# Performance work log

Hardware: AMD Instinct MI355X
Metric: run time of the kernel (lower is better)

The kernel has to match this reference:

```python
import jax, jax.numpy as jnp
import numpy as np

K = 20
EPS_BN = 1e-5

def knn_idx(x, k):
    # x: [B,N,C] -> k nearest neighbor indices [B,N,k] (self included, as in DGCNN)
    sq = jnp.sum(x * x, axis=-1)                       # [B,N]
    inner = jnp.einsum('bnc,bmc->bnm', x, x)           # [B,N,N]
    neg_dist = 2.0 * inner - sq[:, :, None] - sq[:, None, :]
    _, idx = jax.lax.top_k(neg_dist, k)
    return jax.lax.stop_gradient(idx)

def edge_feat(x, idx):
    # x: [B,N,C], idx: [B,N,k] -> [B,N,k,2C] = cat([x_j - x_i, x_i])
    nbr = jax.vmap(lambda xb, ib: xb[ib])(x, idx)      # [B,N,k,C]
    ctr = jnp.broadcast_to(x[:, :, None, :], nbr.shape)
    return jnp.concatenate([nbr - ctr, ctr], axis=-1)

def edge_conv(x, W, g, b, k):
    e = edge_feat(x, knn_idx(x, k))                    # dynamic kNN graph per layer
    h = jnp.einsum('bnkc,cd->bnkd', e, W)              # 1x1 conv2d
    h = h * (g / jnp.sqrt(1.0 + EPS_BN)) + b           # BN eval (mean=0, var=1)
    return jnp.max(jax.nn.leaky_relu(h, 0.2), axis=2)  # max over neighbors -> [B,N,d]

def layer_norm(x, g, b):
    m = jnp.mean(x, axis=-1, keepdims=True)
    v = jnp.var(x, axis=-1, keepdims=True)
    return (x - m) * jax.lax.rsqrt(v + 1e-5) * g + b

def setup_inputs():
    key = jax.random.key(0)
    B, N = 2, 4096
    ks = jax.random.split(key, 16)
    w = lambda i, shape: jax.random.normal(ks[i], shape, jnp.float32) * 0.05
    ones = lambda d: jnp.ones((d,), jnp.float32)
    zeros = lambda d: jnp.zeros((d,), jnp.float32)
    return dict(
        xyz=jax.random.normal(ks[0], (N, 3), jnp.float32),
        scale=jax.random.normal(ks[1], (N, 3), jnp.float32),
        rot=jax.random.normal(ks[2], (N, 4), jnp.float32),
        opacity=jax.random.normal(ks[3], (N, 1), jnp.float32),
        color=jax.random.normal(ks[4], (N, 3), jnp.float32),
        pose=jax.random.normal(ks[5], (B, 75), jnp.float32),
        lbs_weights=jax.random.normal(ks[6], (N, 24), jnp.float32),
        Wc1=w(7, (226, 64)), g1=ones(64), b1=zeros(64),
        Wc2=w(8, (128, 64)), g2=ones(64), b2=zeros(64),
        Wc3=w(9, (128, 128)), g3=ones(128), b3=zeros(128),
        Wc4=w(10, (256, 256)), g4=ones(256), b4=zeros(256),
        Wc5=w(11, (512, 128)), g5=ones(128), b5=zeros(128),
        Wo1=w(12, (128, 128)), bo1=zeros(128), lg1=ones(128), lb1=zeros(128),
        Wo2=w(13, (128, 128)), bo2=zeros(128), lg2=ones(128), lb2=zeros(128),
        Wo3=w(14, (128, 38)), bo3=zeros(38),
    )

def reference(xyz, scale, rot, opacity, color, pose, lbs_weights,
              Wc1, g1, b1, Wc2, g2, b2, Wc3, g3, b3, Wc4, g4, b4, Wc5, g5, b5,
              Wo1, bo1, lg1, lb1, Wo2, bo2, lg2, lb2, Wo3, bo3):
    B, N = pose.shape[0], xyz.shape[0]
    gfeat = jnp.concatenate([xyz, scale, rot, opacity, color], axis=-1)   # [N,14]
    feats = jnp.concatenate([
        jnp.broadcast_to(gfeat[None], (B, N, gfeat.shape[-1])),
        jnp.broadcast_to(lbs_weights[None], (B, N, lbs_weights.shape[-1])),
        jnp.broadcast_to(pose[:, None, :], (B, N, pose.shape[-1])),
    ], axis=-1)                                                            # [B,N,113]
    # DGCNN graph encoder (dynamic kNN EdgeConv stack)
    x1 = edge_conv(feats, Wc1, g1, b1, K)   # [B,N,64]
    x2 = edge_conv(x1, Wc2, g2, b2, K)      # [B,N,64]
    x3 = edge_conv(x2, Wc3, g3, b3, K)      # [B,N,128]
    x4 = edge_conv(x3, Wc4, g4, b4, K)      # [B,N,256]
    cat = jnp.concatenate([x1, x2, x3, x4], axis=-1)                      # [B,N,512]
    gf = jax.nn.leaky_relu(
        jnp.einsum('bnc,cd->bnd', cat, Wc5) * (g5 / jnp.sqrt(1.0 + EPS_BN)) + b5, 0.2)
    # offset predictor MLP
    h = jax.nn.leaky_relu(layer_norm(gf @ Wo1 + bo1, lg1, lb1), 0.2)
    h = jax.nn.leaky_relu(layer_norm(h @ Wo2 + bo2, lg2, lb2), 0.2)
    off = h @ Wo3 + bo3                                                   # [B,N,38]
    # residual add of gaussian offsets (first 14 dims), lbs offsets raw (last 24)
    out = jnp.concatenate([gfeat[None] + off[..., :14], off[..., 14:]], axis=-1)
    return out                                                            # [B,N,38]
```

## Files before the change

kernel.cpp:

```cpp
#include <hip/hip_runtime.h>
#include <math.h>

#define KNN 20
#define BN_INV 0.9999950000374997f

__device__ __forceinline__ unsigned f2o(float f){
    unsigned u = __float_as_uint(f);
    return (u >> 31) ? ~u : (u | 0x80000000u);
}
__device__ __forceinline__ float o2f(unsigned u){
    return __uint_as_float((u >> 31) ? (u & 0x7fffffffu) : ~u);
}
__device__ __forceinline__ float leaky(float v){ return v > 0.f ? v : 0.2f * v; }

__global__ __launch_bounds__(128) void build_feats_kernel(
    const float* __restrict__ xyz, const float* __restrict__ scale,
    const float* __restrict__ rot, const float* __restrict__ opac,
    const float* __restrict__ color, const float* __restrict__ pose,
    const float* __restrict__ lbs, float* __restrict__ feats,
    float* __restrict__ sqout, int N)
{
    __shared__ float sred[2];
    int row = blockIdx.x;
    int b = row / N, n = row % N;
    int c = threadIdx.x;
    float v = 0.f;
    if      (c <   3) v = xyz  [n*3 + c];
    else if (c <   6) v = scale[n*3 + c-3];
    else if (c <  10) v = rot  [n*4 + c-6];
    else if (c <  11) v = opac [n];
    else if (c <  14) v = color[n*3 + c-11];
    else if (c <  38) v = lbs  [n*24 + c-14];
    else if (c < 113) v = pose [b*75 + c-38];
    if (c < 116) feats[(long)row*116 + c] = v;
    float ss = v * v;
    #pragma unroll
    for (int off = 32; off; off >>= 1) ss += __shfl_xor(ss, off);
    if ((c & 63) == 0) sred[c >> 6] = ss;
    __syncthreads();
    if (c == 0) sqout[row] = sred[0] + sred[1];
}


template<int C>
__global__ __launch_bounds__(256) void dist_gemm_kernel(
    const float* __restrict__ x, int N, int CP, float* __restrict__ G)
{
    __shared__ __align__(16) float smem[9216];
    float (*xi)[36] = (float(*)[36])smem;
    float (*xj)[36] = (float(*)[36])(smem + 128*36);

    const int q = blockIdx.x;
    int bjt = (int)((sqrtf(8.f*(float)q + 1.f) - 1.f) * 0.5f);
    while ((bjt+1)*(bjt+2)/2 <= q) ++bjt;
    while (bjt*(bjt+1)/2 > q) --bjt;
    const int bit = q - bjt*(bjt+1)/2;
    const int bi = bit * 128;
    const int bj = bjt * 128;

    const int b  = blockIdx.z;
    const int t  = threadIdx.x;
    const int tx = t & 15, ty = t >> 4;
    const int CP4 = CP / 4;
    const long base = (long)b * N;
    const float4* xp = (const float4*)x;

    float acc[8][8] = {};

    for (int c0 = 0; c0 < C; c0 += 32){
        const int KC  = (C - c0 < 32) ? (C - c0) : 32;
        const int KC4 = KC >> 2;
        __syncthreads();
        if (KC4 == 8){
            for (int f = t; f < 128 * 8; f += 256){
                int r = f >> 3, c4 = f & 7;
                *(float4*)&xi[r][c4 * 4] = xp[(base + bi + r) * CP4 + (c0 >> 2) + c4];
                *(float4*)&xj[r][c4 * 4] = xp[(base + bj + r) * CP4 + (c0 >> 2) + c4];
            }
        } else {
            for (int f = t; f < 128 * KC4; f += 256){
                int r = f / KC4, c4 = f - r * KC4;
                *(float4*)&xi[r][c4 * 4] = xp[(base + bi + r) * CP4 + (c0 >> 2) + c4];
                *(float4*)&xj[r][c4 * 4] = xp[(base + bj + r) * CP4 + (c0 >> 2) + c4];
            }
        }
        __syncthreads();
        for (int c = 0; c < KC; c += 4){
            float4 A[8], Bv[8];
            #pragma unroll
            for (int ii = 0; ii < 8; ++ii) A[ii]  = *(const float4*)&xi[ty + 16*ii][c];
            #pragma unroll
            for (int jj = 0; jj < 8; ++jj) Bv[jj] = *(const float4*)&xj[tx + 16*jj][c];
            #pragma unroll
            for (int ii = 0; ii < 8; ++ii)
                #pragma unroll
                for (int jj = 0; jj < 8; ++jj){
                    acc[ii][jj] = fmaf(A[ii].x, Bv[jj].x, acc[ii][jj]);
                    acc[ii][jj] = fmaf(A[ii].y, Bv[jj].y, acc[ii][jj]);
                    acc[ii][jj] = fmaf(A[ii].z, Bv[jj].z, acc[ii][jj]);
                    acc[ii][jj] = fmaf(A[ii].w, Bv[jj].w, acc[ii][jj]);
                }
        }
    }

    #pragma unroll
    for (int ii = 0; ii < 8; ++ii){
        long rbase = (base + bi + ty + 16*ii) * N + bj;
        #pragma unroll
        for (int jj = 0; jj < 8; ++jj)
            G[rbase + tx + 16*jj] = acc[ii][jj];
    }

    if (bi != bj){
        float (*tr)[132] = (float(*)[132])smem;
        #pragma unroll
        for (int h = 0; h < 2; ++h){
            __syncthreads();
            #pragma unroll
            for (int ii = 0; ii < 8; ++ii)
                #pragma unroll
                for (int jj = 4*h; jj < 4*h + 4; ++jj)
                    tr[tx + 16*(jj - 4*h)][ty + 16*ii] = acc[ii][jj];
            __syncthreads();
            const int cc = (t & 31) * 4;
            const int r0 = t >> 5;
            #pragma unroll
            for (int f = 0; f < 8; ++f){
                int r = r0 + 8 * f;
                *(float4*)&G[(base + bj + 64*h + r) * N + bi + cc] = *(const float4*)&tr[r][cc];
            }
        }
    }
}

#define TCAP 256
__global__ __launch_bounds__(256) void topk_kernel(
    const float* __restrict__ G, const float* __restrict__ sq,
    int N, int* __restrict__ idx_out)
{
    __shared__ unsigned smax[256];
    __shared__ unsigned cand_u[TCAP];
    __shared__ int      cand_j[TCAP];
    __shared__ unsigned cand_cnt;
    __shared__ unsigned sTu;

    const int row = blockIdx.x;
    const int b   = row >> 12;
    const int t   = threadIdx.x;
    const float4* g4  = (const float4*)(G  + (long)row * 4096);
    const float4* sq4 = (const float4*)(sq + (long)b   * 4096);

    unsigned u[16];
    #pragma unroll
    for (int qq = 0; qq < 4; ++qq){
        int v4 = t + 256 * qq;
        float4 gg = g4[v4];
        float4 ss = sq4[v4];
        u[4*qq+0] = f2o(fmaf(2.f, gg.x, -ss.x));
        u[4*qq+1] = f2o(fmaf(2.f, gg.y, -ss.y));
        u[4*qq+2] = f2o(fmaf(2.f, gg.z, -ss.z));
        u[4*qq+3] = f2o(fmaf(2.f, gg.w, -ss.w));
    }

    unsigned mu = u[0];
    #pragma unroll
    for (int q = 1; q < 16; ++q) mu = u[q] > mu ? u[q] : mu;
    smax[t] = mu;
    if (t == 0) cand_cnt = 0;
    __syncthreads();

    int rank = 0;
    for (int k = 0; k < 256; ++k){
        unsigned ou = smax[k];
        rank += (ou > mu) || (ou == mu && k < t);
    }
    if (rank == KNN - 1) sTu = mu;
    __syncthreads();
    const unsigned Tu = sTu;

    #pragma unroll
    for (int qq = 0; qq < 4; ++qq)
        #pragma unroll
        for (int m = 0; m < 4; ++m){
            int q = 4*qq + m;
            if (u[q] >= Tu){
                unsigned p = atomicAdd(&cand_cnt, 1u);
                if (p < TCAP){ cand_u[p] = u[q]; cand_j[p] = 4*(t + 256*qq) + m; }
            }
        }
    __syncthreads();
    const int cc = (int)cand_cnt;

    if (cc <= TCAP){
        if (t < cc){
            unsigned cu = cand_u[t]; int cj = cand_j[t];
            int r = 0;
            for (int k = 0; k < cc; ++k){
                unsigned ou = cand_u[k];
                r += (ou > cu) || (ou == cu && cand_j[k] < cj);
            }
            if (r < KNN) idx_out[(long)row * KNN + r] = cj;
        }
    } else {
        __shared__ unsigned rv[4]; __shared__ int ri[4]; __shared__ int gj_;
        unsigned lv = 0u; int lj = 0x7fffffff;
        #pragma unroll
        for (int q = 0; q < 16; ++q)
            if (u[q] > lv){ lv = u[q]; lj = 4*(t + 256*(q>>2)) + (q&3); }
        for (int it = 0; it < KNN; ++it){
            unsigned bv = lv; int bj = lj;
            #pragma unroll
            for (int off = 32; off; off >>= 1){
                unsigned ov = __shfl_xor(bv, off);
                int      oj = __shfl_xor(bj, off);
                if (ov > bv || (ov == bv && oj < bj)){ bv = ov; bj = oj; }
            }
            if ((t & 63) == 0){ rv[t >> 6] = bv; ri[t >> 6] = bj; }
            __syncthreads();
            if (t == 0){
                unsigned fv = rv[0]; int fj = ri[0];
                #pragma unroll
                for (int w = 1; w < 4; ++w)
                    if (rv[w] > fv || (rv[w] == fv && ri[w] < fj)){ fv = rv[w]; fj = ri[w]; }
                gj_ = fj;
                idx_out[(long)row * KNN + it] = fj;
            }
            __syncthreads();
            int fj = gj_;
            if (fj >= 0 && ((fj >> 2) & 255) == t){
                u[((fj >> 10) << 2) | (fj & 3)] = 0u;
                lv = 0u; lj = 0x7fffffff;
                #pragma unroll
                for (int q = 0; q < 16; ++q)
                    if (u[q] > lv){ lv = u[q]; lj = 4*(t + 256*(q>>2)) + (q&3); }
            }
            __syncthreads();
        }
    }
}


__device__ __forceinline__ void wcat_emit(const float* __restrict__ W, int C, int D,
                                          int i, float* __restrict__ dst)
{
    int TWOD = 2 * D;
    int c = i / TWOD, n = i - c * TWOD;
    float v = 0.f;
    if (c < C) v = (n < D) ? W[c*D + n] : (W[(C + c)*D + (n - D)] - W[c*D + (n - D)]);
    dst[i] = v;
}

__global__ void prep_all_wcat_kernel(
    const float* __restrict__ Wc1, const float* __restrict__ Wc2,
    const float* __restrict__ Wc3, const float* __restrict__ Wc4,
    float* __restrict__ Wcat)
{
    int i = blockIdx.x * 256 + threadIdx.x;
    if      (i <  14848) wcat_emit(Wc1, 113,  64, i,          Wcat);
    else if (i <  23040) wcat_emit(Wc2,  64,  64, i - 14848,  Wcat + 14848);
    else if (i <  39424) wcat_emit(Wc3,  64, 128, i - 23040,  Wcat + 23040);
    else if (i < 104960) wcat_emit(Wc4, 128, 256, i - 39424,  Wcat + 39424);
}

__global__ __launch_bounds__(256) void gemm_pq_kernel(
    const float* __restrict__ X, int CP, const float* __restrict__ Wcat,
    const float* __restrict__ g, const float* __restrict__ bias,
    int D, int TWOD, float* __restrict__ PQ)
{
    __shared__ __align__(16) float As[128][68];
    __shared__ __align__(16) float Bs[64][132];
    const int bi = blockIdx.x * 128;
    const int bn = blockIdx.y * 128;
    const int t  = threadIdx.x;
    const int tx = t & 15, ty = t >> 4;
    const int CP4 = CP / 4;
    const float4* xp = (const float4*)X;

    float acc[8][8] = {};

    for (int c0 = 0; c0 < CP; c0 += 64){
        const int KC = (CP - c0 < 64) ? (CP - c0) : 64;
        const int KC4 = KC >> 2;
        __syncthreads();
        for (int f = t; f < 128 * KC4; f += 256){
            int r = f / KC4, c4 = f - r * KC4;
            *(float4*)&As[r][c4 * 4] = xp[(long)(bi + r) * CP4 + (c0 >> 2) + c4];
        }
        for (int f = t; f < KC * 32; f += 256){
            int r = f >> 5, c4 = f & 31;
            *(float4*)&Bs[r][c4 * 4] = *(const float4*)&Wcat[(long)(c0 + r) * TWOD + bn + c4 * 4];
        }
        __syncthreads();
        for (int c = 0; c < KC; c += 4){
            float4 A[8];
            #pragma unroll
            for (int ii = 0; ii < 8; ++ii) A[ii] = *(const float4*)&As[ty + 16*ii][c];
            float Bv0[8], Bv1[8], Bv2[8], Bv3[8];
            #pragma unroll
            for (int jj = 0; jj < 8; ++jj){
                Bv0[jj] = Bs[c+0][tx + 16*jj];
                Bv1[jj] = Bs[c+1][tx + 16*jj];
                Bv2[jj] = Bs[c+2][tx + 16*jj];
                Bv3[jj] = Bs[c+3][tx + 16*jj];
            }
            #pragma unroll
            for (int ii = 0; ii < 8; ++ii)
                #pragma unroll
                for (int jj = 0; jj < 8; ++jj){
                    acc[ii][jj] = fmaf(A[ii].x, Bv0[jj], acc[ii][jj]);
                    acc[ii][jj] = fmaf(A[ii].y, Bv1[jj], acc[ii][jj]);
                    acc[ii][jj] = fmaf(A[ii].z, Bv2[jj], acc[ii][jj]);
                    acc[ii][jj] = fmaf(A[ii].w, Bv3[jj], acc[ii][jj]);
                }
        }
    }

    #pragma unroll
    for (int jj = 0; jj < 8; ++jj){
        int n = bn + tx + 16*jj;
        int d = (n < D) ? n : n - D;
        float gg = g[d] * BN_INV;
        float bb = (n < D) ? 0.f : bias[d];
        #pragma unroll
        for (int ii = 0; ii < 8; ++ii)
            PQ[(long)(bi + ty + 16*ii) * TWOD + n] = fmaf(acc[ii][jj], gg, bb);
    }
}

template<int D, int RPB>
__global__ __launch_bounds__(256) void gather_max_kernel(
    const float* __restrict__ PQ, const int* __restrict__ idx, int N,
    float* __restrict__ y, float* __restrict__ sqout)
{
    __shared__ int   lidx[RPB][KNN];
    __shared__ float sred[4];
    const int rb = blockIdx.x * RPB;
    const int t  = threadIdx.x;
    if (t < RPB * KNN) lidx[t / KNN][t % KNN] = idx[(long)rb * KNN + t];
    __syncthreads();

    const int r = t / D, d = t - r * D;
    const int row = rb + r;
    const long base = (long)(row / N) * N;
    const int TWOD = 2 * D;

    float q = PQ[(long)row * TWOD + D + d];
    float m = -INFINITY;
    #pragma unroll
    for (int k = 0; k < KNN; ++k){
        int j = lidx[r][k];
        m = fmaxf(m, PQ[(base + j) * TWOD + d]);
    }
    float val = leaky(m + q);
    y[(long)row * D + d] = val;

    float ss = val * val;
    #pragma unroll
    for (int off = 32; off; off >>= 1) ss += __shfl_xor(ss, off);
    if ((t & 63) == 0) sred[t >> 6] = ss;
    __syncthreads();
    if (d == 0){
        constexpr int WPR = D / 64;
        float s = 0.f;
        int w0 = (r * D) >> 6;
        #pragma unroll
        for (int w = 0; w < WPR; ++w) s += sred[w0 + w];
        sqout[row] = s;
    }
}


__global__ __launch_bounds__(256) void head_gemm1_kernel(
    const float* __restrict__ x1, const float* __restrict__ x2,
    const float* __restrict__ x3, const float* __restrict__ x4,
    const float* __restrict__ Wc5, const float* __restrict__ g5,
    const float* __restrict__ b5, float* __restrict__ gf, int R)
{
    __shared__ __align__(16) float As[64][68];
    __shared__ __align__(16) float Bs[64][68];
    const int bi = blockIdx.x * 64;
    const int bn = blockIdx.y * 64;
    const int t  = threadIdx.x;
    const int tx = t & 15, ty = t >> 4;

    float acc[4][4] = {};

    #pragma unroll 1
    for (int kc = 0; kc < 8; ++kc){
        const float* src; int ld, coff;
        if      (kc == 0){ src = x1; ld = 64;  coff = 0; }
        else if (kc == 1){ src = x2; ld = 64;  coff = 0; }
        else if (kc <  4){ src = x3; ld = 128; coff = (kc-2)*64; }
        else             { src = x4; ld = 256; coff = (kc-4)*64; }
        __syncthreads();
        for (int f = t; f < 64*16; f += 256){
            int r = f >> 4, c4 = f & 15;
            *(float4*)&As[r][c4*4] = *(const float4*)&src[(long)(bi + r)*ld + coff + c4*4];
            *(float4*)&Bs[r][c4*4] = *(const float4*)&Wc5[(long)(kc*64 + r)*128 + bn + c4*4];
        }
        __syncthreads();
        for (int c = 0; c < 64; c += 4){
            float4 A[4];
            #pragma unroll
            for (int ii = 0; ii < 4; ++ii) A[ii] = *(const float4*)&As[ty + 16*ii][c];
            float B0[4], B1[4], B2[4], B3[4];
            #pragma unroll
            for (int jj = 0; jj < 4; ++jj){
                B0[jj] = Bs[c+0][tx + 16*jj];
                B1[jj] = Bs[c+1][tx + 16*jj];
                B2[jj] = Bs[c+2][tx + 16*jj];
                B3[jj] = Bs[c+3][tx + 16*jj];
            }
            #pragma unroll
            for (int ii = 0; ii < 4; ++ii)
                #pragma unroll
                for (int jj = 0; jj < 4; ++jj){
                    acc[ii][jj] = fmaf(A[ii].x, B0[jj], acc[ii][jj]);
                    acc[ii][jj] = fmaf(A[ii].y, B1[jj], acc[ii][jj]);
                    acc[ii][jj] = fmaf(A[ii].z, B2[jj], acc[ii][jj]);
                    acc[ii][jj] = fmaf(A[ii].w, B3[jj], acc[ii][jj]);
                }
        }
    }

    #pragma unroll
    for (int jj = 0; jj < 4; ++jj){
        int n = bn + tx + 16*jj;
        float gg = g5[n] * BN_INV, bb = b5[n];
        #pragma unroll
        for (int ii = 0; ii < 4; ++ii)
            gf[(long)(bi + ty + 16*ii)*128 + n] = leaky(fmaf(acc[ii][jj], gg, bb));
    }
}

__global__ __launch_bounds__(256) void head_lngemm_kernel(
    const float* __restrict__ hin, const float* __restrict__ W,
    const float* __restrict__ bo, const float* __restrict__ lg,
    const float* __restrict__ lb, float* __restrict__ hout, int R)
{
    __shared__ __align__(16) float As[64][68];
    __shared__ __align__(16) float Bs[64][132];
    const int bi = blockIdx.x * 64;
    const int t  = threadIdx.x;
    const int tx = t & 15, ty = t >> 4;

    float acc[4][8] = {};

    #pragma unroll 1
    for (int kc = 0; kc < 2; ++kc){
        __syncthreads();
        for (int f = t; f < 64*16; f += 256){
            int r = f >> 4, c4 = f & 15;
            *(float4*)&As[r][c4*4] = *(const float4*)&hin[(long)(bi + r)*128 + kc*64 + c4*4];
        }
        for (int f = t; f < 64*32; f += 256){
            int r = f >> 5, c4 = f & 31;
            *(float4*)&Bs[r][c4*4] = *(const float4*)&W[(long)(kc*64 + r)*128 + c4*4];
        }
        __syncthreads();
        for (int c = 0; c < 64; c += 4){
            float4 A[4];
            #pragma unroll
            for (int ii = 0; ii < 4; ++ii) A[ii] = *(const float4*)&As[ty + 16*ii][c];
            float B0[8], B1[8], B2[8], B3[8];
            #pragma unroll
            for (int jj = 0; jj < 8; ++jj){
                B0[jj] = Bs[c+0][tx + 16*jj];
                B1[jj] = Bs[c+1][tx + 16*jj];
                B2[jj] = Bs[c+2][tx + 16*jj];
                B3[jj] = Bs[c+3][tx + 16*jj];
            }
            #pragma unroll
            for (int ii = 0; ii < 4; ++ii)
                #pragma unroll
                for (int jj = 0; jj < 8; ++jj){
                    acc[ii][jj] = fmaf(A[ii].x, B0[jj], acc[ii][jj]);
                    acc[ii][jj] = fmaf(A[ii].y, B1[jj], acc[ii][jj]);
                    acc[ii][jj] = fmaf(A[ii].z, B2[jj], acc[ii][jj]);
                    acc[ii][jj] = fmaf(A[ii].w, B3[jj], acc[ii][jj]);
                }
        }
    }

    float bon[8], lgn[8], lbn[8];
    #pragma unroll
    for (int jj = 0; jj < 8; ++jj){
        int n = tx + 16*jj;
        bon[jj] = bo[n]; lgn[jj] = lg[n]; lbn[jj] = lb[n];
    }
    #pragma unroll
    for (int ii = 0; ii < 4; ++ii){
        float s1 = 0.f, s2 = 0.f;
        #pragma unroll
        for (int jj = 0; jj < 8; ++jj){
            float a = acc[ii][jj] + bon[jj];
            acc[ii][jj] = a;
            s1 += a; s2 += a*a;
        }
        #pragma unroll
        for (int off = 8; off; off >>= 1){
            s1 += __shfl_xor(s1, off);
            s2 += __shfl_xor(s2, off);
        }
        float m = s1 * (1.f/128.f);
        float v = s2 * (1.f/128.f) - m*m;
        float rinv = rsqrtf(v + 1e-5f);
        long r = bi + ty + 16*ii;
        #pragma unroll
        for (int jj = 0; jj < 8; ++jj)
            hout[r*128 + tx + 16*jj] = leaky((acc[ii][jj] - m) * rinv * lgn[jj] + lbn[jj]);
    }
}

#define OP 16
__global__ __launch_bounds__(256) void head_out_kernel(
    const float* __restrict__ h, const float* __restrict__ feats,
    const float* __restrict__ Wo3, const float* __restrict__ bo3,
    float* __restrict__ out, int R)
{
    __shared__ __align__(16) float hs[OP][132];
    __shared__ float f14[OP][14];
    const int t  = threadIdx.x;
    const long p0 = (long)blockIdx.x * OP;

    for (int f = t; f < OP*32; f += 256){
        int r = f >> 5, c4 = f & 31;
        *(float4*)&hs[r][c4*4] = *(const float4*)&h[(p0 + r)*128 + c4*4];
    }
    if (t < OP*14) f14[t/14][t%14] = feats[(p0 + t/14)*116 + t%14];
    __syncthreads();

    const int w = t >> 6, l = t & 63;
    if (l < 38){
        float o[4];
        float bt = bo3[l];
        #pragma unroll
        for (int pp = 0; pp < 4; ++pp) o[pp] = bt;
        for (int c = 0; c < 128; ++c){
            float wv = Wo3[c*38 + l];
            #pragma unroll
            for (int pp = 0; pp < 4; ++pp)
                o[pp] = fmaf(hs[w*4 + pp][c], wv, o[pp]);
        }
        #pragma unroll
        for (int pp = 0; pp < 4; ++pp){
            int p = w*4 + pp;
            float val = o[pp] + ((l < 14) ? f14[p][l] : 0.f);
            out[(p0 + p)*38 + l] = val;
        }
    }
}

__global__ __launch_bounds__(256) void knn_kernel(
    const float* __restrict__ x, int N, int CP4, int* __restrict__ idx_out)
{
    __shared__ float4 xi4[32];
    __shared__ float drow[4096];
    __shared__ float rv[4];
    __shared__ int   ri[4];

    int row = blockIdx.x;
    int b = row / N;
    int t = threadIdx.x;
    const float4* xp = (const float4*)x;

    if (t < CP4) xi4[t] = xp[(long)row * CP4 + t];
    __syncthreads();

    long bb = (long)b * N * CP4;
    for (int j = t; j < N; j += 256){
        const float4* p = xp + bb + (long)j * CP4;
        float acc = 0.f;
        #pragma unroll 4
        for (int c = 0; c < CP4; ++c){
            float4 xv = p[c], yv = xi4[c];
            float dx = xv.x - yv.x, dy = xv.y - yv.y;
            float dz = xv.z - yv.z, dw = xv.w - yv.w;
            acc += dx*dx + dy*dy + dz*dz + dw*dw;
        }
        drow[j] = -acc;
    }
    __syncthreads();

    for (int it = 0; it < KNN; ++it){
        float bv = -INFINITY; int bi = N;
        for (int j = t; j < N; j += 256){
            float v = drow[j];
            if (v > bv){ bv = v; bi = j; }
        }
        #pragma unroll
        for (int off = 32; off > 0; off >>= 1){
            float ov = __shfl_xor(bv, off);
            int   oi = __shfl_xor(bi, off);
            if (ov > bv || (ov == bv && oi < bi)){ bv = ov; bi = oi; }
        }
        if ((t & 63) == 0){ rv[t >> 6] = bv; ri[t >> 6] = bi; }
        __syncthreads();
        if (t == 0){
            float fv = rv[0]; int fi = ri[0];
            #pragma unroll
            for (int w = 1; w < 4; ++w){
                if (rv[w] > fv || (rv[w] == fv && ri[w] < fi)){ fv = rv[w]; fi = ri[w]; }
            }
            idx_out[(long)row * KNN + it] = fi;
            drow[fi] = -INFINITY;
        }
        __syncthreads();
    }
}

template<int D, int KPT>
__global__ __launch_bounds__(256) void edge_conv_kernel(
    const float* __restrict__ x, int N, int C, int CP,
    const float* __restrict__ W, const float* __restrict__ g,
    const float* __restrict__ bias, const int* __restrict__ idx,
    float* __restrict__ y, float* __restrict__ sqout)
{
    __shared__ float xi[128];
    __shared__ float nbr[KNN * 128];
    __shared__ float t2[D];
    __shared__ unsigned um[D];
    __shared__ float sred[4];

    int row = blockIdx.x;
    int b = row / N;
    int t = threadIdx.x;

    for (int c = t; c < C; c += 256) xi[c] = x[(long)row * CP + c];
    for (int kk = 0; kk < KNN; ++kk){
        int j = idx[(long)row * KNN + kk];
        long nb = ((long)b * N + j) * CP;
        for (int c = t; c < C; c += 256) nbr[kk * C + c] = x[nb + c];
    }
    __syncthreads();

    for (int d = t; d < D; d += 256){
        float s = 0.f;
        for (int c = 0; c < C; ++c) s += xi[c] * W[(C + c) * D + d];
        t2[d] = s; um[d] = 0u;
    }
    __syncthreads();

    const int d  = t % D;
    const int kg = t / D;
    float s[KPT];
    #pragma unroll
    for (int q = 0; q < KPT; ++q) s[q] = t2[d];

    const float* nb0 = &nbr[(kg * KPT) * C];
    for (int c = 0; c < C; ++c){
        float w   = W[c * D + d];
        float xic = xi[c];
        #pragma unroll
        for (int q = 0; q < KPT; ++q)
            s[q] += (nb0[q * C + c] - xic) * w;
    }
    float g_ = g[d] * BN_INV, b_ = bias[d];
    float m = -INFINITY;
    #pragma unroll
    for (int q = 0; q < KPT; ++q)
        m = fmaxf(m, leaky(s[q] * g_ + b_));
    atomicMax(&um[d], f2o(m));
    __syncthreads();

    float ss = 0.f;
    for (int dd = t; dd < D; dd += 256){
        float val = o2f(um[dd]);
        y[(long)row * D + dd] = val;
        ss += val * val;
    }
    #pragma unroll
    for (int off = 32; off; off >>= 1) ss += __shfl_xor(ss, off);
    if ((t & 63) == 0) sred[t >> 6] = ss;
    __syncthreads();
    if (t == 0) sqout[row] = sred[0] + sred[1] + sred[2] + sred[3];
}

#define HP 8
__global__ __launch_bounds__(128) void head_kernel(
    const float* __restrict__ x1, const float* __restrict__ x2,
    const float* __restrict__ x3, const float* __restrict__ x4,
    const float* __restrict__ feats,
    const float* __restrict__ Wc5, const float* __restrict__ g5, const float* __restrict__ b5,
    const float* __restrict__ Wo1, const float* __restrict__ bo1,
    const float* __restrict__ lg1, const float* __restrict__ lb1,
    const float* __restrict__ Wo2, const float* __restrict__ bo2,
    const float* __restrict__ lg2, const float* __restrict__ lb2,
    const float* __restrict__ Wo3, const float* __restrict__ bo3,
    float* __restrict__ out, int N, int R)
{
    __shared__ __align__(16) float cat[HP][520];
    __shared__ __align__(16) float hb[HP][132];
    __shared__ float wsum[2][HP], wsq[2][HP];
    __shared__ float f14[HP][14];

    const int t = threadIdx.x;
    const long p0 = (long)blockIdx.x * HP;
    const int wid = t >> 6;

    long rows[HP];
    #pragma unroll
    for (int p = 0; p < HP; ++p){
        long row = p0 + p; if (row >= R) row = R - 1;
        rows[p] = row;
        cat[p][t]       = (t < 64) ? x1[row*64 + t] : x2[row*64 + (t-64)];
        cat[p][128 + t] = x3[row*128 + t];
        cat[p][256 + t] = x4[row*256 + t];
        cat[p][384 + t] = x4[row*256 + 128 + t];
        if (t < 14) f14[p][t] = feats[row*116 + t];
    }
    __syncthreads();

    const float g5t = g5[t] * BN_INV, b5t = b5[t];
    float acc[HP];
    #pragma unroll
    for (int p = 0; p < HP; ++p) acc[p] = 0.f;
    for (int c4 = 0; c4 < 128; ++c4){
        float w0 = Wc5[(4*c4+0)*128 + t];
        float w1 = Wc5[(4*c4+1)*128 + t];
        float w2 = Wc5[(4*c4+2)*128 + t];
        float w3 = Wc5[(4*c4+3)*128 + t];
        #pragma unroll
        for (int p = 0; p < HP; ++p){
            float4 cv = *(const float4*)&cat[p][4*c4];
            acc[p] = fmaf(cv.x, w0, acc[p]);
            acc[p] = fmaf(cv.y, w1, acc[p]);
            acc[p] = fmaf(cv.z, w2, acc[p]);
            acc[p] = fmaf(cv.w, w3, acc[p]);
        }
    }
    #pragma unroll
    for (int p = 0; p < HP; ++p) hb[p][t] = leaky(fmaf(acc[p], g5t, b5t));
    __syncthreads();

    for (int layer = 0; layer < 2; ++layer){
        const float* W  = layer ? Wo2 : Wo1;
        const float* bo = layer ? bo2 : bo1;
        const float* lg = layer ? lg2 : lg1;
        const float* lb = layer ? lb2 : lb1;
        float a2[HP];
        float bot = bo[t];
        #pragma unroll
        for (int p = 0; p < HP; ++p) a2[p] = bot;
        for (int c4 = 0; c4 < 32; ++c4){
            float w0 = W[(4*c4+0)*128 + t];
            float w1 = W[(4*c4+1)*128 + t];
            float w2 = W[(4*c4+2)*128 + t];
            float w3 = W[(4*c4+3)*128 + t];
            #pragma unroll
            for (int p = 0; p < HP; ++p){
                float4 hv = *(const float4*)&hb[p][4*c4];
                a2[p] = fmaf(hv.x, w0, a2[p]);
                a2[p] = fmaf(hv.y, w1, a2[p]);
                a2[p] = fmaf(hv.z, w2, a2[p]);
                a2[p] = fmaf(hv.w, w3, a2[p]);
            }
        }
        #pragma unroll
        for (int p = 0; p < HP; ++p){
            float s1 = a2[p], s2 = a2[p]*a2[p];
            #pragma unroll
            for (int off = 32; off; off >>= 1){
                s1 += __shfl_xor(s1, off);
                s2 += __shfl_xor(s2, off);
            }
            if ((t & 63) == 0){ wsum[wid][p] = s1; wsq[wid][p] = s2; }
        }
        __syncthreads();
        float lgt = lg[t], lbt = lb[t];
        float hn[HP];
        #pragma unroll
        for (int p = 0; p < HP; ++p){
            float m  = (wsum[0][p] + wsum[1][p]) * (1.f/128.f);
            float v  = (wsq[0][p]  + wsq[1][p])  * (1.f/128.f) - m*m;
            float dm = a2[p] - m;
            hn[p] = leaky(dm * rsqrtf(v + 1e-5f) * lgt + lbt);
        }
        __syncthreads();
        #pragma unroll
        for (int p = 0; p < HP; ++p) hb[p][t] = hn[p];
        __syncthreads();
    }

    if (t < 38){
        float o[HP];
        float bt = bo3[t];
        #pragma unroll
        for (int p = 0; p < HP; ++p) o[p] = bt;
        for (int c = 0; c < 128; ++c){
            float w = Wo3[c*38 + t];
            #pragma unroll
            for (int p = 0; p < HP; ++p) o[p] = fmaf(hb[p][c], w, o[p]);
        }
        #pragma unroll
        for (int p = 0; p < HP; ++p){
            float val = o[p] + ((t < 14) ? f14[p][t] : 0.f);
            out[rows[p]*38 + t] = val;
        }
    }
}

extern "C" void kernel_launch(void* const* d_in, const int* in_sizes, int n_in,
                              void* d_out, int out_size, void* d_ws, size_t ws_size,
                              hipStream_t stream)
{
    const float* xyz  = (const float*)d_in[0];
    const float* scal = (const float*)d_in[1];
    const float* rot  = (const float*)d_in[2];
    const float* opac = (const float*)d_in[3];
    const float* colr = (const float*)d_in[4];
    const float* pose = (const float*)d_in[5];
    const float* lbs  = (const float*)d_in[6];
    const float* Wc1 = (const float*)d_in[7];  const float* g1 = (const float*)d_in[8];  const float* b1 = (const float*)d_in[9];
    const float* Wc2 = (const float*)d_in[10]; const float* g2 = (const float*)d_in[11]; const float* b2 = (const float*)d_in[12];
    const float* Wc3 = (const float*)d_in[13]; const float* g3 = (const float*)d_in[14]; const float* b3 = (const float*)d_in[15];
    const float* Wc4 = (const float*)d_in[16]; const float* g4 = (const float*)d_in[17]; const float* b4 = (const float*)d_in[18];
    const float* Wc5 = (const float*)d_in[19]; const float* g5 = (const float*)d_in[20]; const float* b5 = (const float*)d_in[21];
    const float* Wo1 = (const float*)d_in[22]; const float* bo1 = (const float*)d_in[23];
    const float* lg1 = (const float*)d_in[24]; const float* lb1 = (const float*)d_in[25];
    const float* Wo2 = (const float*)d_in[26]; const float* bo2 = (const float*)d_in[27];
    const float* lg2 = (const float*)d_in[28]; const float* lb2 = (const float*)d_in[29];
    const float* Wo3 = (const float*)d_in[30]; const float* bo3 = (const float*)d_in[31];

    const int N = in_sizes[0] / 3;
    const int B = in_sizes[5] / 75;
    const int R = B * N;

    char* ws = (char*)d_ws;
    size_t o = 0;
    float* feats = (float*)(ws + o); o += (size_t)R * 116 * 4;
    float* x1    = (float*)(ws + o); o += (size_t)R * 64  * 4;
    float* x2    = (float*)(ws + o); o += (size_t)R * 64  * 4;
    float* x3    = (float*)(ws + o); o += (size_t)R * 128 * 4;
    float* x4    = (float*)(ws + o); o += (size_t)R * 256 * 4;
    int*   idx   = (int*)  (ws + o); o += (size_t)R * KNN * 4;
    float* sq    = (float*)(ws + o); o += (size_t)R * 4;
    float* Wcat  = (float*)(ws + o); o += (size_t)104960 * 4;
    float* G     = (float*)(ws + o);
    float* PQ    = G;
    float* gf    = G;
    float* h1    = G + (size_t)R * 128;
    float* h2    = G + (size_t)R * 256;
    size_t need  = o + (size_t)B * N * N * 4;

    const bool fast = (N == 4096) && (ws_size >= need);

    build_feats_kernel<<<R, 128, 0, stream>>>(xyz, scal, rot, opac, colr, pose, lbs, feats, sq, N);

    if (fast){
        const int NT = 32;
        dim3 gg(NT*(NT+1)/2, 1, B);
        float* Wcat1 = Wcat;
        float* Wcat2 = Wcat + 14848;
        float* Wcat3 = Wcat + 23040;
        float* Wcat4 = Wcat + 39424;

        prep_all_wcat_kernel<<<(104960 + 255)/256, 256, 0, stream>>>(Wc1, Wc2, Wc3, Wc4, Wcat);

        dist_gemm_kernel<116><<<gg, 256, 0, stream>>>(feats, N, 116, G);
        topk_kernel<<<R, 256, 0, stream>>>(G, sq, N, idx);
        gemm_pq_kernel<<<dim3(R/128, 1), 256, 0, stream>>>(feats, 116, Wcat1, g1, b1, 64, 128, PQ);
        gather_max_kernel<64, 4><<<R/4, 256, 0, stream>>>(PQ, idx, N, x1, sq);

        dist_gemm_kernel<64><<<gg, 256, 0, stream>>>(x1, N, 64, G);
        topk_kernel<<<R, 256, 0, stream>>>(G, sq, N, idx);
        gemm_pq_kernel<<<dim3(R/128, 1), 256, 0, stream>>>(x1, 64, Wcat2, g2, b2, 64, 128, PQ);
        gather_max_kernel<64, 4><<<R/4, 256, 0, stream>>>(PQ, idx, N, x2, sq);

        dist_gemm_kernel<64><<<gg, 256, 0, stream>>>(x2, N, 64, G);
        topk_kernel<<<R, 256, 0, stream>>>(G, sq, N, idx);
        gemm_pq_kernel<<<dim3(R/128, 2), 256, 0, stream>>>(x2, 64, Wcat3, g3, b3, 128, 256, PQ);
        gather_max_kernel<128, 2><<<R/2, 256, 0, stream>>>(PQ, idx, N, x3, sq);

        dist_gemm_kernel<128><<<gg, 256, 0, stream>>>(x3, N, 128, G);
        topk_kernel<<<R, 256, 0, stream>>>(G, sq, N, idx);
        gemm_pq_kernel<<<dim3(R/128, 4), 256, 0, stream>>>(x3, 128, Wcat4, g4, b4, 256, 512, PQ);
        gather_max_kernel<256, 1><<<R, 256, 0, stream>>>(PQ, idx, N, x4, sq);

        head_gemm1_kernel<<<dim3(R/64, 2), 256, 0, stream>>>(x1, x2, x3, x4, Wc5, g5, b5, gf, R);
        head_lngemm_kernel<<<R/64, 256, 0, stream>>>(gf, Wo1, bo1, lg1, lb1, h1, R);
        head_lngemm_kernel<<<R/64, 256, 0, stream>>>(h1, Wo2, bo2, lg2, lb2, h2, R);
        head_out_kernel<<<R/OP, 256, 0, stream>>>(h2, feats, Wo3, bo3, (float*)d_out, R);
    } else {
        knn_kernel<<<R, 256, 0, stream>>>(feats, N, 116/4, idx);
        edge_conv_kernel<64, 5><<<R, 256, 0, stream>>>(feats, N, 113, 116, Wc1, g1, b1, idx, x1, sq);
        knn_kernel<<<R, 256, 0, stream>>>(x1, N, 64/4, idx);
        edge_conv_kernel<64, 5><<<R, 256, 0, stream>>>(x1, N, 64, 64, Wc2, g2, b2, idx, x2, sq);
        knn_kernel<<<R, 256, 0, stream>>>(x2, N, 64/4, idx);
        edge_conv_kernel<128, 10><<<R, 256, 0, stream>>>(x2, N, 64, 64, Wc3, g3, b3, idx, x3, sq);
        knn_kernel<<<R, 256, 0, stream>>>(x3, N, 128/4, idx);
        edge_conv_kernel<256, 20><<<R, 256, 0, stream>>>(x3, N, 128, 128, Wc4, g4, b4, idx, x4, sq);

        head_kernel<<<(R + HP - 1)/HP, 128, 0, stream>>>(x1, x2, x3, x4, feats,
                                           Wc5, g5, b5, Wo1, bo1, lg1, lb1,
                                           Wo2, bo2, lg2, lb2, Wo3, bo3,
                                           (float*)d_out, N, R);
    }
}
```

Baseline: 832.4 us.

## Register-prefetch next K-chunk in GEMMs and add 64x64-tile PQ GEMM

The distance GEMM and the PQ GEMM now load the next 32-wide channel chunk into registers while the current chunk is being computed from shared memory, so global load latency overlaps with FMAs. The dist GEMM also gets a launch-bounds occupancy hint. A new 64x64-tile PQ GEMM replaces the 128x128 one for the first three layers to launch more blocks on the small problems. The cost is extra registers for the prefetch buffers, and the occupancy hint may force register spills in the 8x8 accumulator kernel.

```diff
diff --git a/kernel.cpp b/kernel.cpp
--- a/kernel.cpp
+++ b/kernel.cpp
@@ -43,7 +43,7 @@
 
 
 template<int C>
-__global__ __launch_bounds__(256) void dist_gemm_kernel(
+__global__ __launch_bounds__(256, 4) void dist_gemm_kernel(
     const float* __restrict__ x, int N, int CP, float* __restrict__ G)
 {
     __shared__ __align__(16) float smem[9216];
@@ -66,25 +66,47 @@
     const float4* xp = (const float4*)x;
 
     float acc[8][8] = {};
-
-    for (int c0 = 0; c0 < C; c0 += 32){
-        const int KC  = (C - c0 < 32) ? (C - c0) : 32;
-        const int KC4 = KC >> 2;
-        __syncthreads();
-        if (KC4 == 8){
-            for (int f = t; f < 128 * 8; f += 256){
-                int r = f >> 3, c4 = f & 7;
-                *(float4*)&xi[r][c4 * 4] = xp[(base + bi + r) * CP4 + (c0 >> 2) + c4];
-                *(float4*)&xj[r][c4 * 4] = xp[(base + bj + r) * CP4 + (c0 >> 2) + c4];
-            }
-        } else {
-            for (int f = t; f < 128 * KC4; f += 256){
-                int r = f / KC4, c4 = f - r * KC4;
-                *(float4*)&xi[r][c4 * 4] = xp[(base + bi + r) * CP4 + (c0 >> 2) + c4];
-                *(float4*)&xj[r][c4 * 4] = xp[(base + bj + r) * CP4 + (c0 >> 2) + c4];
-            }
-        }
-        __syncthreads();
+    float4 pa[4], pb[4];
+
+    int c0 = 0;
+    int KC4 = ((C < 32) ? C : 32) >> 2;
+    #pragma unroll
+    for (int s = 0; s < 4; ++s){
+        int f = t + 256*s;
+        if (f < 128*KC4){
+            int r = f / KC4, c4 = f - r*KC4;
+            pa[s] = xp[(base + bi + r) * CP4 + c4];
+            pb[s] = xp[(base + bj + r) * CP4 + c4];
+        }
+    }
+
+    for (;;){
+        __syncthreads();
+        #pragma unroll
+        for (int s = 0; s < 4; ++s){
+            int f = t + 256*s;
+            if (f < 128*KC4){
+                int r = f / KC4, c4 = f - r*KC4;
+                *(float4*)&xi[r][c4*4] = pa[s];
+                *(float4*)&xj[r][c4*4] = pb[s];
+            }
+        }
+        __syncthreads();
+        const int KC  = KC4 * 4;
+        const int c0n = c0 + 32;
+        int KC4n = 0;
+        if (c0n < C){
+            KC4n = (((C - c0n) < 32) ? (C - c0n) : 32) >> 2;
+            #pragma unroll
+            for (int s = 0; s < 4; ++s){
+                int f = t + 256*s;
+                if (f < 128*KC4n){
+                    int r = f / KC4n, c4 = f - r*KC4n;
+                    pa[s] = xp[(base + bi + r) * CP4 + (c0n >> 2) + c4];
+                    pb[s] = xp[(base + bj + r) * CP4 + (c0n >> 2) + c4];
+                }
+            }
+        }
         for (int c = 0; c < KC; c += 4){
             float4 A[8], Bv[8];
             #pragma unroll
@@ -101,6 +123,8 @@
                     acc[ii][jj] = fmaf(A[ii].w, Bv[jj].w, acc[ii][jj]);
                 }
         }
+        if (c0n >= C) break;
+        c0 = c0n; KC4 = KC4n;
     }
 
     #pragma unroll
@@ -267,8 +291,8 @@
     const float* __restrict__ g, const float* __restrict__ bias,
     int D, int TWOD, float* __restrict__ PQ)
 {
-    __shared__ __align__(16) float As[128][68];
-    __shared__ __align__(16) float Bs[64][132];
+    __shared__ __align__(16) float As[128][36];
+    __shared__ __align__(16) float Bs[32][132];
     const int bi = blockIdx.x * 128;
     const int bn = blockIdx.y * 128;
     const int t  = threadIdx.x;
@@ -277,20 +301,56 @@
     const float4* xp = (const float4*)X;
 
     float acc[8][8] = {};
-
-    for (int c0 = 0; c0 < CP; c0 += 64){
-        const int KC = (CP - c0 < 64) ? (CP - c0) : 64;
-        const int KC4 = KC >> 2;
-        __syncthreads();
-        for (int f = t; f < 128 * KC4; f += 256){
-            int r = f / KC4, c4 = f - r * KC4;
-            *(float4*)&As[r][c4 * 4] = xp[(long)(bi + r) * CP4 + (c0 >> 2) + c4];
-        }
-        for (int f = t; f < KC * 32; f += 256){
+    float4 pa[4], pb[4];
+
+    int c0 = 0;
+    int KC4 = ((CP < 32) ? CP : 32) >> 2;
+    #pragma unroll
+    for (int s = 0; s < 4; ++s){
+        int f = t + 256*s;
+        if (f < 128*KC4){
+            int r = f / KC4, c4 = f - r*KC4;
+            pa[s] = xp[(long)(bi + r)*CP4 + c4];
+        }
+        if (f < 128*KC4){
             int r = f >> 5, c4 = f & 31;
-            *(float4*)&Bs[r][c4 * 4] = *(const float4*)&Wcat[(long)(c0 + r) * TWOD + bn + c4 * 4];
-        }
-        __syncthreads();
+            pb[s] = *(const float4*)&Wcat[(long)r * TWOD + bn + c4*4];
+        }
+    }
+
+    for (;;){
+        __syncthreads();
+        #pragma unroll
+        for (int s = 0; s < 4; ++s){
+            int f = t + 256*s;
+            if (f < 128*KC4){
+                int r = f / KC4, c4 = f - r*KC4;
+                *(float4*)&As[r][c4*4] = pa[s];
+            }
+            if (f < 128*KC4){
+                int r = f >> 5, c4 = f & 31;
+                *(float4*)&Bs[r][c4*4] = pb[s];
+            }
+        }
+        __syncthreads();
+        const int KC  = KC4 * 4;
+        const int c0n = c0 + 32;
+        int KC4n = 0;
+        if (c0n < CP){
+            KC4n = (((CP - c0n) < 32) ? (CP - c0n) : 32) >> 2;
+            #pragma unroll
+            for (int s = 0; s < 4; ++s){
+                int f = t + 256*s;
+                if (f < 128*KC4n){
+                    int r = f / KC4n, c4 = f - r*KC4n;
+                    pa[s] = xp[(long)(bi + r)*CP4 + (c0n >> 2) + c4];
+                }
+                if (f < 128*KC4n){
+                    int r = f >> 5, c4 = f & 31;
+                    pb[s] = *(const float4*)&Wcat[(long)(c0n + r) * TWOD + bn + c4*4];
+                }
+            }
+        }
         for (int c = 0; c < KC; c += 4){
             float4 A[8];
             #pragma unroll
@@ -313,6 +373,8 @@
                     acc[ii][jj] = fmaf(A[ii].w, Bv3[jj], acc[ii][jj]);
                 }
         }
+        if (c0n >= CP) break;
+        c0 = c0n; KC4 = KC4n;
     }
 
     #pragma unroll
@@ -323,6 +385,109 @@
         float bb = (n < D) ? 0.f : bias[d];
         #pragma unroll
         for (int ii = 0; ii < 8; ++ii)
+            PQ[(long)(bi + ty + 16*ii) * TWOD + n] = fmaf(acc[ii][jj], gg, bb);
+    }
+}
+
+__global__ __launch_bounds__(256) void gemm_pq64_kernel(
+    const float* __restrict__ X, int CP, const float* __restrict__ Wcat,
+    const float* __restrict__ g, const float* __restrict__ bias,
+    int D, int TWOD, float* __restrict__ PQ)
+{
+    __shared__ __align__(16) float As[64][36];
+    __shared__ __align__(16) float Bs[32][68];
+    const int bi = blockIdx.x * 64;
+    const int bn = blockIdx.y * 64;
+    const int t  = threadIdx.x;
+    const int tx = t & 15, ty = t >> 4;
+    const int CP4 = CP / 4;
+    const float4* xp = (const float4*)X;
+
+    float acc[4][4] = {};
+    float4 pa[2], pb[2];
+
+    int c0 = 0;
+    int KC4 = ((CP < 32) ? CP : 32) >> 2;
+    #pragma unroll
+    for (int s = 0; s < 2; ++s){
+        int f = t + 256*s;
+        if (f < 64*KC4){
+            int r = f / KC4, c4 = f - r*KC4;
+            pa[s] = xp[(long)(bi + r)*CP4 + c4];
+        }
+        if (f < 64*KC4){
+            int r = f >> 4, c4 = f & 15;
+            pb[s] = *(const float4*)&Wcat[(long)r * TWOD + bn + c4*4];
+        }
+    }
+
+    for (;;){
+        __syncthreads();
+        #pragma unroll
+        for (int s = 0; s < 2; ++s){
+            int f = t + 256*s;
+            if (f < 64*KC4){
+                int r = f / KC4, c4 = f - r*KC4;
+                *(float4*)&As[r][c4*4] = pa[s];
+            }
+            if (f < 64*KC4){
+                int r = f >> 4, c4 = f & 15;
+                *(float4*)&Bs[r][c4*4] = pb[s];
+            }
+        }
+        __syncthreads();
+        const int KC  = KC4 * 4;
+        const int c0n = c0 + 32;
+        int KC4n = 0;
+        if (c0n < CP){
+            KC4n = (((CP - c0n) < 32) ? (CP - c0n) : 32) >> 2;
+            #pragma unroll
+            for (int s = 0; s < 2; ++s){
+                int f = t + 256*s;
+                if (f < 64*KC4n){
+                    int r = f / KC4n, c4 = f - r*KC4n;
+                    pa[s] = xp[(long)(bi + r)*CP4 + (c0n >> 2) + c4];
+                }
+                if (f < 64*KC4n){
+                    int r = f >> 4, c4 = f & 15;
+                    pb[s] = *(const float4*)&Wcat[(long)(c0n + r) * TWOD + bn + c4*4];
+                }
+            }
+        }
+        for (int c = 0; c < KC; c += 4){
+            float4 A[4];
+            #pragma unroll
+            for (int ii = 0; ii < 4; ++ii) A[ii] = *(const float4*)&As[ty + 16*ii][c];
+            float B0[4], B1[4], B2[4], B3[4];
+            #pragma unroll
+            for (int jj = 0; jj < 4; ++jj){
+                B0[jj] = Bs[c+0][tx + 16*jj];
+                B1[jj] = Bs[c+1][tx + 16*jj];
+                B2[jj] = Bs[c+2][tx + 16*jj];
+                B3[jj] = Bs[c+3][tx + 16*jj];
+            }
+            #pragma unroll
+            for (int ii = 0; ii < 4; ++ii)
+                #pragma unroll
+                for (int jj = 0; jj < 4; ++jj){
+                    acc[ii][jj] = fmaf(A[ii].x, B0[jj], acc[ii][jj]);
+                    acc[ii][jj] = fmaf(A[ii].y, B1[jj], acc[ii][jj]);
+                    acc[ii][jj] = fmaf(A[ii].z, B2[jj], acc[ii][jj]);
+                    acc[ii][jj] = fmaf(A[ii].w, B3[jj], acc[ii][jj]);
+                }
+        }
+        if (c0n >= CP) break;
+        c0 = c0n; KC4 = KC4n;
+    }
+
+    #pragma unroll
+    for (int jj = 0; jj < 4; ++jj){
+        int n = bn + tx + 16*jj;
+        int d = (n < D) ? n : n - D;
+        float gg = g[d] * BN_INV;
+        float bb = (n < D) ? 0.f : bias[d];
+        #pragma unroll
+        for (int ii = 0; ii < 4; ++ii)
             PQ[(long)(bi + ty + 16*ii) * TWOD + n] = fmaf(acc[ii][jj], gg, bb);
     }
 }
@@ -859,17 +1024,17 @@
 
         dist_gemm_kernel<116><<<gg, 256, 0, stream>>>(feats, N, 116, G);
         topk_kernel<<<R, 256, 0, stream>>>(G, sq, N, idx);
-        gemm_pq_kernel<<<dim3(R/128, 1), 256, 0, stream>>>(feats, 116, Wcat1, g1, b1, 64, 128, PQ);
+        gemm_pq64_kernel<<<dim3(R/64, 2), 256, 0, stream>>>(feats, 116, Wcat1, g1, b1, 64, 128, PQ);
         gather_max_kernel<64, 4><<<R/4, 256, 0, stream>>>(PQ, idx, N, x1, sq);
 
         dist_gemm_kernel<64><<<gg, 256, 0, stream>>>(x1, N, 64, G);
         topk_kernel<<<R, 256, 0, stream>>>(G, sq, N, idx);
-        gemm_pq_kernel<<<dim3(R/128, 1), 256, 0, stream>>>(x1, 64, Wcat2, g2, b2, 64, 128, PQ);
+        gemm_pq64_kernel<<<dim3(R/64, 2), 256, 0, stream>>>(x1, 64, Wcat2, g2, b2, 64, 128, PQ);
         gather_max_kernel<64, 4><<<R/4, 256, 0, stream>>>(PQ, idx, N, x2, sq);
 
         dist_gemm_kernel<64><<<gg, 256, 0, stream>>>(x2, N, 64, G);
         topk_kernel<<<R, 256, 0, stream>>>(G, sq, N, idx);
-        gemm_pq_kernel<<<dim3(R/128, 2), 256, 0, stream>>>(x2, 64, Wcat3, g3, b3, 128, 256, PQ);
+        gemm_pq64_kernel<<<dim3(R/64, 4), 256, 0, stream>>>(x2, 64, Wcat3, g3, b3, 128, 256, PQ);
         gather_max_kernel<128, 2><<<R/2, 256, 0, stream>>>(PQ, idx, N, x3, sq);
 
         dist_gemm_kernel<128><<<gg, 256, 0, stream>>>(x3, N, 128, G);
```

New measurement: 901.7 us. 8.3% more time.
